# Optimization experiments

Measured on AMD Instinct MI355X. Metric: run time of the kernel, lower is better.

## Reference

```python
import jax, jax.numpy as jnp
import numpy as np

N = 50000        # node_num
E = 1600000      # num edges (avg degree 32)
IN_DIM = 128
OUT_DIM = 64
SLOPE = 0.1      # leaky relu slope_ratio
EPS = 1e-12


def setup_inputs() -> dict:
    key = jax.random.key(0)
    k0, k1, k2, k3 = jax.random.split(key, 4)
    x = jax.random.normal(k0, (N, IN_DIM), dtype=jnp.float32)
    edge_index = jax.random.randint(k1, (2, E), 0, N, dtype=jnp.int64)
    # Linear(in_dim, out_dim) params
    W = jax.random.normal(k2, (OUT_DIM, IN_DIM), dtype=jnp.float32) * (1.0 / np.sqrt(IN_DIM))
    b = jnp.zeros((OUT_DIM,), dtype=jnp.float32)
    # attention vector a: [2*out_dim, 1], kaiming-normal-ish init
    a = jax.random.normal(k3, (2 * OUT_DIM, 1), dtype=jnp.float32) * np.sqrt(2.0 / (2 * OUT_DIM))
    return {"x": x, "edge_index": edge_index, "W": W, "b": b, "a": a}


def reference(x, edge_index, W, b, a):
    # new_embeddings = Linear(x)
    new = x @ W.T + b                          # [N, OUT_DIM]
    src = edge_index[0]
    dst = edge_index[1]
    # cat(new[src], new[dst]) @ a  ==  new[src]@a_src + new[dst]@a_dst (avoids [E, 2*OUT] intermediate)
    a_src = a[:OUT_DIM, 0]                     # [OUT_DIM]
    a_dst = a[OUT_DIM:, 0]                     # [OUT_DIM]
    score = new[src] @ a_src + new[dst] @ a_dst  # [E]
    e = jnp.exp(jax.nn.leaky_relu(score, SLOPE))  # [E]
    # spmm(A, ones) -> per-row sum of edge weights; spmm(A, new) -> weighted aggregation
    row_sum = jax.ops.segment_sum(e, src, num_segments=N)                 # [N]
    results = jax.ops.segment_sum(e[:, None] * new[dst], src, num_segments=N)  # [N, OUT_DIM]
    return results / (row_sum[:, None] + EPS)
```

## Files before the change

### kernel.cpp

```cpp
#include <hip/hip_runtime.h>
#include <hip/hip_bf16.h>

#define NN    50000
#define EE    1600000
#define IND   128
#define OUTD  64
#define SLOPE 0.1f

#define BSH    5
#define BW     32
#define NB     1564
#define NFINE  1568
#define CAP    1408
#define CAPT   6
#define CSH    8
#define NC     196
#define CAP1   8832
#define NBLK1  500
#define CHUNK1 (EE / NBLK1)
#define NSPLIT 4
#define SCAP   (CAP1 / NSPLIT)
#define NLIN   (NN / 16)

typedef __attribute__((ext_vector_type(8))) short short8;
typedef __attribute__((ext_vector_type(4))) float float4v;

union SMem {
    struct {
        ushort xs[16 * 136];
        ushort wt[64 * 136];
        float  newt[16 * 68];
    } lin;
    int h[NC];
};

__global__ __launch_bounds__(256) void fused_lincoarse_kernel(
    const float* __restrict__ x, const float* __restrict__ W,
    const float* __restrict__ bias, const float* __restrict__ a,
    const int* __restrict__ ei, int* __restrict__ gcur1,
    unsigned* __restrict__ ebuf1,
    ushort* __restrict__ nbuf2, float* __restrict__ s_src, float* __restrict__ s_dst)
{
    __shared__ SMem sm;
    const int tid = threadIdx.x;

    if (blockIdx.x < NBLK1) {
        int* h = sm.h;
        for (int i = tid; i < NC; i += 256) h[i] = 0;
        __syncthreads();
        const int base = blockIdx.x * CHUNK1;
        const int4* s4p = (const int4*)(ei + base);
        for (int i = tid; i < CHUNK1 / 4; i += 256) {
            int4 s4 = s4p[i];
            atomicAdd(&h[s4.x >> CSH], 1);
            atomicAdd(&h[s4.y >> CSH], 1);
            atomicAdd(&h[s4.z >> CSH], 1);
            atomicAdd(&h[s4.w >> CSH], 1);
        }
        __syncthreads();
        for (int i = tid; i < NC; i += 256) {
            int c = h[i];
            if (c) h[i] = i * CAP1 + atomicAdd(&gcur1[i * 16], c);
        }
        __syncthreads();
        const int4* d4p = (const int4*)(ei + EE + base);
        for (int i = tid; i < CHUNK1 / 4; i += 256) {
            int4 s4 = s4p[i];
            int4 d4 = d4p[i];
            int p0 = atomicAdd(&h[s4.x >> CSH], 1);
            int p1 = atomicAdd(&h[s4.y >> CSH], 1);
            int p2 = atomicAdd(&h[s4.z >> CSH], 1);
            int p3 = atomicAdd(&h[s4.w >> CSH], 1);
            ebuf1[p0] = ((unsigned)(s4.x & 255) << 16) | (unsigned)d4.x;
            ebuf1[p1] = ((unsigned)(s4.y & 255) << 16) | (unsigned)d4.y;
            ebuf1[p2] = ((unsigned)(s4.z & 255) << 16) | (unsigned)d4.z;
            ebuf1[p3] = ((unsigned)(s4.w & 255) << 16) | (unsigned)d4.w;
        }
        return;
    }

    const int node0 = (blockIdx.x - NBLK1) * 16;
    const float4* W4 = (const float4*)W;
    #pragma unroll
    for (int i = 0; i < 8; ++i) {
        int idx = tid + i * 256;
        float4 wv = W4[idx];
        int n = idx >> 5, k = (idx & 31) * 4;
        ushort4 pk; __hip_bfloat16 h;
        h = __float2bfloat16(wv.x); pk.x = *(ushort*)&h;
        h = __float2bfloat16(wv.y); pk.y = *(ushort*)&h;
        h = __float2bfloat16(wv.z); pk.z = *(ushort*)&h;
        h = __float2bfloat16(wv.w); pk.w = *(ushort*)&h;
        *(ushort4*)&sm.lin.wt[n * 136 + k] = pk;
    }
    const float4* x4 = (const float4*)(x + (size_t)node0 * IND);
    #pragma unroll
    for (int i = 0; i < 2; ++i) {
        int idx = tid + i * 256;
        float4 xv = x4[idx];
        int r = idx >> 5, cc = (idx & 31) * 4;
        ushort4 pk; __hip_bfloat16 h;
        h = __float2bfloat16(xv.x); pk.x = *(ushort*)&h;
        h = __float2bfloat16(xv.y); pk.y = *(ushort*)&h;
        h = __float2bfloat16(xv.z); pk.z = *(ushort*)&h;
        h = __float2bfloat16(xv.w); pk.w = *(ushort*)&h;
        *(ushort4*)&sm.lin.xs[r * 136 + cc] = pk;
    }
    __syncthreads();

    const int w    = tid >> 6;
    const int lane = tid & 63;
    const int q    = lane >> 4;
    const int m16  = lane & 15;
    float4v acc = {0.f, 0.f, 0.f, 0.f};
    #pragma unroll
    for (int kk = 0; kk < IND; kk += 32) {
        short8 af = *(const short8*)&sm.lin.xs[m16 * 136 + kk + q * 8];
        short8 bf = *(const short8*)&sm.lin.wt[(w * 16 + m16) * 136 + kk + q * 8];
        acc = __builtin_amdgcn_mfma_f32_16x16x32_bf16(af, bf, acc, 0, 0, 0);
    }
    const float bv = bias[w * 16 + m16];
    #pragma unroll
    for (int r = 0; r < 4; ++r)
        sm.lin.newt[(q * 4 + r) * 68 + w * 16 + m16] = acc[r] + bv;
    __syncthreads();

    const int nl = tid >> 4;
    const int jg = tid & 15;
    const int j0 = jg * 4;
    float4 va = *(const float4*)&sm.lin.newt[nl * 68 + j0];
    const int n = node0 + nl;
    ushort4 pk;
    { __hip_bfloat16 h;
      h = __float2bfloat16(va.x); pk.x = *(ushort*)&h;
      h = __float2bfloat16(va.y); pk.y = *(ushort*)&h;
      h = __float2bfloat16(va.z); pk.z = *(ushort*)&h;
      h = __float2bfloat16(va.w); pk.w = *(ushort*)&h; }
    *(ushort4*)&nbuf2[(size_t)n * OUTD + j0] = pk;

    float ss = va.x * a[j0]        + va.y * a[j0 + 1]
             + va.z * a[j0 + 2]    + va.w * a[j0 + 3];
    float sd = va.x * a[OUTD + j0]     + va.y * a[OUTD + j0 + 1]
             + va.z * a[OUTD + j0 + 2] + va.w * a[OUTD + j0 + 3];
    #pragma unroll
    for (int m = 1; m < 16; m <<= 1) {
        ss += __shfl_xor(ss, m, 64);
        sd += __shfl_xor(sd, m, 64);
    }
    if (jg == 0) { s_src[n] = ss; s_dst[n] = sd; }
}

__global__ __launch_bounds__(256) void finebin_kernel(
    const unsigned* __restrict__ ebuf1, const int* __restrict__ gcur1,
    int* __restrict__ gcur2, unsigned* __restrict__ ebuf2)
{
    __shared__ unsigned stage[SCAP];
    __shared__ int h[8], lofs[8], grun[8], cur[8];
    const int tid = threadIdx.x;
    const int c   = blockIdx.x >> 2;
    const int sp  = blockIdx.x & 3;
    const int cnt1 = gcur1[c * 16];
    const int seg  = (cnt1 + NSPLIT - 1) / NSPLIT;
    const int lo   = sp * seg;
    const int m    = max(0, min(cnt1, lo + seg) - lo);
    if (tid < 8) h[tid] = 0;
    __syncthreads();
    const unsigned* eb = ebuf1 + (size_t)c * CAP1 + lo;
    for (int i = tid; i < m; i += 256)
        atomicAdd(&h[eb[i] >> 21], 1);
    __syncthreads();
    if (tid == 0) {
        int run = 0;
        #pragma unroll
        for (int f = 0; f < 8; ++f) { lofs[f] = run; run += h[f]; }
    }
    __syncthreads();
    if (tid < 8) {
        cur[tid]  = lofs[tid];
        grun[tid] = atomicAdd(&gcur2[(c * 8 + tid) * 16], h[tid]);
    }
    __syncthreads();
    for (int i = tid; i < m; i += 256) {
        unsigned e = eb[i];
        int pos = atomicAdd(&cur[e >> 21], 1);
        stage[pos] = (((e >> 16) & 31u) << 16) | (e & 0xFFFFu);
    }
    __syncthreads();
    #pragma unroll 1
    for (int f = 0; f < 8; ++f) {
        const int cf = h[f];
        unsigned* dst = ebuf2 + (size_t)(c * 8 + f) * CAP + grun[f];
        const unsigned* sp2 = stage + lofs[f];
        for (int i = tid; i < cf; i += 256) dst[i] = sp2[i];
    }
}

__global__ __launch_bounds__(256) void aggregate_kernel(
    const unsigned* __restrict__ ebuf, const int* __restrict__ gcur,
    const ushort* __restrict__ nbuf2,
    const float* __restrict__ s_src, const float* __restrict__ s_dst,
    float* __restrict__ out)
{
    __shared__ uint2 pairs[CAP];
    __shared__ float ssL[BW];
    __shared__ int cntL[BW], ofs[BW], cur[BW];
    const int tid  = threadIdx.x;
    const int wid  = tid >> 6;
    const int lane = tid & 63;
    const int b    = blockIdx.x;
    const int n0   = b << BSH;
    const uint2* __restrict__ nbufq = (const uint2*)nbuf2;

    if (tid < BW) {
        int n = n0 + tid;
        ssL[tid]  = (n < NN) ? s_src[n] : 0.f;
        cntL[tid] = 0;
    }
    __syncthreads();

    const int cnt = gcur[b * 16];
    const unsigned* eb = ebuf + (size_t)b * CAP;

    unsigned er[CAPT]; float evr[CAPT];
    #pragma unroll
    for (int k = 0; k < CAPT; ++k) {
        int i = tid + k * 256;
        if (i < cnt) {
            unsigned e = eb[i];
            er[k] = e;
            int d  = e & 0xFFFFu;
            int ln = e >> 16;
            float sc = ssL[ln] + s_dst[d];
            float lr = sc > 0.f ? sc : SLOPE * sc;
            evr[k] = __expf(lr);
            atomicAdd(&cntL[ln], 1);
        }
    }
    __syncthreads();

    if (wid == 0) {
        int c = (lane < BW) ? cntL[lane] : 0;
        int sc = c;
        #pragma unroll
        for (int m = 1; m < BW; m <<= 1) {
            int v = __shfl_up(sc, m, 64);
            if (lane >= m) sc += v;
        }
        if (lane < BW) { ofs[lane] = sc - c; cur[lane] = sc - c; }
    }
    __syncthreads();

    #pragma unroll
    for (int k = 0; k < CAPT; ++k) {
        int i = tid + k * 256;
        if (i < cnt) {
            int ln = er[k] >> 16;
            int pos = atomicAdd(&cur[ln], 1);
            pairs[pos] = make_uint2(er[k] & 0xFFFFu, __float_as_uint(evr[k]));
        }
    }
    __syncthreads();

    const int e16 = lane >> 4;
    const int c16 = lane & 15;

    #pragma unroll 1
    for (int t = 0; t < BW / 4; ++t) {
        const int ln  = wid * (BW / 4) + t;
        const int beg = ofs[ln];
        const int len = cntL[ln];

        float a0 = 0.f, a1 = 0.f, a2 = 0.f, a3 = 0.f, es = 0.f;
        int j = 0;
        for (; j + 32 <= len; j += 32) {
            uint2 pA = pairs[beg + j + 0  + e16];
            uint2 pB = pairs[beg + j + 4  + e16];
            uint2 pC = pairs[beg + j + 8  + e16];
            uint2 pD = pairs[beg + j + 12 + e16];
            uint2 pE = pairs[beg + j + 16 + e16];
            uint2 pF = pairs[beg + j + 20 + e16];
            uint2 pG = pairs[beg + j + 24 + e16];
            uint2 pH = pairs[beg + j + 28 + e16];
            uint2 gA = nbufq[pA.x * 16 + c16];
            uint2 gB = nbufq[pB.x * 16 + c16];
            uint2 gC = nbufq[pC.x * 16 + c16];
            uint2 gD = nbufq[pD.x * 16 + c16];
            uint2 gE = nbufq[pE.x * 16 + c16];
            uint2 gF = nbufq[pF.x * 16 + c16];
            uint2 gG = nbufq[pG.x * 16 + c16];
            uint2 gH = nbufq[pH.x * 16 + c16];
            float fA = __uint_as_float(pA.y), fB = __uint_as_float(pB.y);
            float fC = __uint_as_float(pC.y), fD = __uint_as_float(pD.y);
            float fE = __uint_as_float(pE.y), fF = __uint_as_float(pF.y);
            float fG = __uint_as_float(pG.y), fH = __uint_as_float(pH.y);
            es += (fA + fB + fC + fD) + (fE + fF + fG + fH);
            a0 = fmaf(fA, __uint_as_float(gA.x << 16), a0);
            a1 = fmaf(fA, __uint_as_float(gA.x & 0xFFFF0000u), a1);
            a2 = fmaf(fA, __uint_as_float(gA.y << 16), a2);
            a3 = fmaf(fA, __uint_as_float(gA.y & 0xFFFF0000u), a3);
            a0 = fmaf(fB, __uint_as_float(gB.x << 16), a0);
            a1 = fmaf(fB, __uint_as_float(gB.x & 0xFFFF0000u), a1);
            a2 = fmaf(fB, __uint_as_float(gB.y << 16), a2);
            a3 = fmaf(fB, __uint_as_float(gB.y & 0xFFFF0000u), a3);
            a0 = fmaf(fC, __uint_as_float(gC.x << 16), a0);
            a1 = fmaf(fC, __uint_as_float(gC.x & 0xFFFF0000u), a1);
            a2 = fmaf(fC, __uint_as_float(gC.y << 16), a2);
            a3 = fmaf(fC, __uint_as_float(gC.y & 0xFFFF0000u), a3);
            a0 = fmaf(fD, __uint_as_float(gD.x << 16), a0);
            a1 = fmaf(fD, __uint_as_float(gD.x & 0xFFFF0000u), a1);
            a2 = fmaf(fD, __uint_as_float(gD.y << 16), a2);
            a3 = fmaf(fD, __uint_as_float(gD.y & 0xFFFF0000u), a3);
            a0 = fmaf(fE, __uint_as_float(gE.x << 16), a0);
            a1 = fmaf(fE, __uint_as_float(gE.x & 0xFFFF0000u), a1);
            a2 = fmaf(fE, __uint_as_float(gE.y << 16), a2);
            a3 = fmaf(fE, __uint_as_float(gE.y & 0xFFFF0000u), a3);
            a0 = fmaf(fF, __uint_as_float(gF.x << 16), a0);
            a1 = fmaf(fF, __uint_as_float(gF.x & 0xFFFF0000u), a1);
            a2 = fmaf(fF, __uint_as_float(gF.y << 16), a2);
            a3 = fmaf(fF, __uint_as_float(gF.y & 0xFFFF0000u), a3);
            a0 = fmaf(fG, __uint_as_float(gG.x << 16), a0);
            a1 = fmaf(fG, __uint_as_float(gG.x & 0xFFFF0000u), a1);
            a2 = fmaf(fG, __uint_as_float(gG.y << 16), a2);
            a3 = fmaf(fG, __uint_as_float(gG.y & 0xFFFF0000u), a3);
            a0 = fmaf(fH, __uint_as_float(gH.x << 16), a0);
            a1 = fmaf(fH, __uint_as_float(gH.x & 0xFFFF0000u), a1);
            a2 = fmaf(fH, __uint_as_float(gH.y << 16), a2);
            a3 = fmaf(fH, __uint_as_float(gH.y & 0xFFFF0000u), a3);
        }
        for (; j + 16 <= len; j += 16) {
            uint2 pA = pairs[beg + j + 0  + e16];
            uint2 pB = pairs[beg + j + 4  + e16];
            uint2 pC = pairs[beg + j + 8  + e16];
            uint2 pD = pairs[beg + j + 12 + e16];
            uint2 gA = nbufq[pA.x * 16 + c16];
            uint2 gB = nbufq[pB.x * 16 + c16];
            uint2 gC = nbufq[pC.x * 16 + c16];
            uint2 gD = nbufq[pD.x * 16 + c16];
            float fA = __uint_as_float(pA.y), fB = __uint_as_float(pB.y);
            float fC = __uint_as_float(pC.y), fD = __uint_as_float(pD.y);
            es += fA + fB + fC + fD;
            a0 = fmaf(fA, __uint_as_float(gA.x << 16), a0);
            a1 = fmaf(fA, __uint_as_float(gA.x & 0xFFFF0000u), a1);
            a2 = fmaf(fA, __uint_as_float(gA.y << 16), a2);
            a3 = fmaf(fA, __uint_as_float(gA.y & 0xFFFF0000u), a3);
            a0 = fmaf(fB, __uint_as_float(gB.x << 16), a0);
            a1 = fmaf(fB, __uint_as_float(gB.x & 0xFFFF0000u), a1);
            a2 = fmaf(fB, __uint_as_float(gB.y << 16), a2);
            a3 = fmaf(fB, __uint_as_float(gB.y & 0xFFFF0000u), a3);
            a0 = fmaf(fC, __uint_as_float(gC.x << 16), a0);
            a1 = fmaf(fC, __uint_as_float(gC.x & 0xFFFF0000u), a1);
            a2 = fmaf(fC, __uint_as_float(gC.y << 16), a2);
            a3 = fmaf(fC, __uint_as_float(gC.y & 0xFFFF0000u), a3);
            a0 = fmaf(fD, __uint_as_float(gD.x << 16), a0);
            a1 = fmaf(fD, __uint_as_float(gD.x & 0xFFFF0000u), a1);
            a2 = fmaf(fD, __uint_as_float(gD.y << 16), a2);
            a3 = fmaf(fD, __uint_as_float(gD.y & 0xFFFF0000u), a3);
        }
        for (; j < len; j += 4) {
            int idx = j + e16;
            uint2 p = pairs[beg + min(idx, len - 1)];
            float f = (idx < len) ? __uint_as_float(p.y) : 0.f;
            uint2 g = nbufq[p.x * 16 + c16];
            es += f;
            a0 = fmaf(f, __uint_as_float(g.x << 16), a0);
            a1 = fmaf(f, __uint_as_float(g.x & 0xFFFF0000u), a1);
            a2 = fmaf(f, __uint_as_float(g.y << 16), a2);
            a3 = fmaf(f, __uint_as_float(g.y & 0xFFFF0000u), a3);
        }
        es += __shfl_xor(es, 16, 64); es += __shfl_xor(es, 32, 64);
        a0 += __shfl_xor(a0, 16, 64); a0 += __shfl_xor(a0, 32, 64);
        a1 += __shfl_xor(a1, 16, 64); a1 += __shfl_xor(a1, 32, 64);
        a2 += __shfl_xor(a2, 16, 64); a2 += __shfl_xor(a2, 32, 64);
        a3 += __shfl_xor(a3, 16, 64); a3 += __shfl_xor(a3, 32, 64);
        const int n = n0 + ln;
        if (e16 == 0 && n < NN) {
            float inv = 1.f / (es + 1e-12f);
            float4 o = make_float4(a0 * inv, a1 * inv, a2 * inv, a3 * inv);
            *(float4*)&out[(size_t)n * OUTD + c16 * 4] = o;
        }
    }
}

extern "C" void kernel_launch(void* const* d_in, const int* in_sizes, int n_in,
                              void* d_out, int out_size, void* d_ws, size_t ws_size,
                              hipStream_t stream) {
    const float* x  = (const float*)d_in[0];
    const int*   ei = (const int*)d_in[1];
    const float* W  = (const float*)d_in[2];
    const float* b  = (const float*)d_in[3];
    const float* a  = (const float*)d_in[4];
    float* out = (float*)d_out;

    ushort*   nbuf2 = (ushort*)d_ws;
    float*    s_src = (float*)(nbuf2 + (size_t)NN * OUTD);
    float*    s_dst = s_src + NN;
    int*      gcur1 = (int*)(s_dst + NN);
    int*      gcur2 = gcur1 + NC * 16;
    unsigned* ebuf1 = (unsigned*)(gcur2 + NFINE * 16);
    unsigned* ebuf2 = ebuf1 + (size_t)NC * CAP1;

    hipMemsetAsync(gcur1, 0, (NC + NFINE) * 16 * sizeof(int), stream);
    fused_lincoarse_kernel<<<NBLK1 + NLIN, 256, 0, stream>>>(
        x, W, b, a, ei, gcur1, ebuf1, nbuf2, s_src, s_dst);
    finebin_kernel<<<NC * NSPLIT, 256, 0, stream>>>(ebuf1, gcur1, gcur2, ebuf2);
    aggregate_kernel<<<NB, 256, 0, stream>>>(ebuf2, gcur2, nbuf2, s_src, s_dst, out);
}
```

Measured before the change: 145.3 us.

## Bin edges directly into fine 32-node buckets, dropping the two-pass finebin kernel

The coarse-then-fine two-stage edge binning is replaced by a single pass in the fused kernel that histograms edges straight into the 1568 fine buckets and scatters them into the per-bucket buffers that aggregate consumes. This removes the finebin launch, the intermediate ebuf1 write and read, and one global counter array. Source int4 loads are also cached in registers between the count and scatter passes. In exchange each block touches many more shared histogram entries and global atomics (1568 instead of 196 per block), and global writes become more scattered.

Result: slower. 171.1 us (+17.7%).

```diff
diff --git a/kernel.cpp b/kernel.cpp
--- a/kernel.cpp
+++ b/kernel.cpp
@@ -10,16 +10,11 @@
 #define BSH    5
 #define BW     32
 #define NB     1564
-#define NFINE  1568
+#define NFB    1568
 #define CAP    1408
 #define CAPT   6
-#define CSH    8
-#define NC     196
-#define CAP1   8832
 #define NBLK1  500
 #define CHUNK1 (EE / NBLK1)
-#define NSPLIT 4
-#define SCAP   (CAP1 / NSPLIT)
 #define NLIN   (NN / 16)
 
 typedef __attribute__((ext_vector_type(8))) short short8;
@@ -31,14 +26,14 @@
         ushort wt[64 * 136];
         float  newt[16 * 68];
     } lin;
-    int h[NC];
+    int h[NFB];
 };
 
 __global__ __launch_bounds__(256) void fused_lincoarse_kernel(
     const float* __restrict__ x, const float* __restrict__ W,
     const float* __restrict__ bias, const float* __restrict__ a,
-    const int* __restrict__ ei, int* __restrict__ gcur1,
-    unsigned* __restrict__ ebuf1,
+    const int* __restrict__ ei, int* __restrict__ gcur,
+    unsigned* __restrict__ ebuf,
     ushort* __restrict__ nbuf2, float* __restrict__ s_src, float* __restrict__ s_dst)
 {
     __shared__ SMem sm;
@@ -46,35 +41,45 @@
 
     if (blockIdx.x < NBLK1) {
         int* h = sm.h;
-        for (int i = tid; i < NC; i += 256) h[i] = 0;
+        for (int i = tid; i < NFB; i += 256) h[i] = 0;
         __syncthreads();
         const int base = blockIdx.x * CHUNK1;
         const int4* s4p = (const int4*)(ei + base);
-        for (int i = tid; i < CHUNK1 / 4; i += 256) {
-            int4 s4 = s4p[i];
-            atomicAdd(&h[s4.x >> CSH], 1);
-            atomicAdd(&h[s4.y >> CSH], 1);
-            atomicAdd(&h[s4.z >> CSH], 1);
-            atomicAdd(&h[s4.w >> CSH], 1);
+        int4 sst[4];
+        #pragma unroll
+        for (int k = 0; k < 4; ++k) {
+            int i = tid + k * 256;
+            if (i < CHUNK1 / 4) {
+                int4 s4 = s4p[i];
+                sst[k] = s4;
+                atomicAdd(&h[s4.x >> BSH], 1);
+                atomicAdd(&h[s4.y >> BSH], 1);
+                atomicAdd(&h[s4.z >> BSH], 1);
+                atomicAdd(&h[s4.w >> BSH], 1);
+            }
         }
         __syncthreads();
-        for (int i = tid; i < NC; i += 256) {
+        for (int i = tid; i < NFB; i += 256) {
             int c = h[i];
-            if (c) h[i] = i * CAP1 + atomicAdd(&gcur1[i * 16], c);
+            if (c) h[i] = i * CAP + atomicAdd(&gcur[i * 16], c);
         }
         __syncthreads();
         const int4* d4p = (const int4*)(ei + EE + base);
-        for (int i = tid; i < CHUNK1 / 4; i += 256) {
-            int4 s4 = s4p[i];
-            int4 d4 = d4p[i];
-            int p0 = atomicAdd(&h[s4.x >> CSH], 1);
-            int p1 = atomicAdd(&h[s4.y >> CSH], 1);
-            int p2 = atomicAdd(&h[s4.z >> CSH], 1);
-            int p3 = atomicAdd(&h[s4.w >> CSH], 1);
-            ebuf1[p0] = ((unsigned)(s4.x & 255) << 16) | (unsigned)d4.x;
-            ebuf1[p1] = ((unsigned)(s4.y & 255) << 16) | (unsigned)d4.y;
-            ebuf1[p2] = ((unsigned)(s4.z & 255) << 16) | (unsigned)d4.z;
-            ebuf1[p3] = ((unsigned)(s4.w & 255) << 16) | (unsigned)d4.w;
+        #pragma unroll
+        for (int k = 0; k < 4; ++k) {
+            int i = tid + k * 256;
+            if (i < CHUNK1 / 4) {
+                int4 s4 = sst[k];
+                int4 d4 = d4p[i];
+                int p0 = atomicAdd(&h[s4.x >> BSH], 1);
+                int p1 = atomicAdd(&h[s4.y >> BSH], 1);
+                int p2 = atomicAdd(&h[s4.z >> BSH], 1);
+                int p3 = atomicAdd(&h[s4.w >> BSH], 1);
+                ebuf[p0] = ((unsigned)(s4.x & 31) << 16) | (unsigned)d4.x;
+                ebuf[p1] = ((unsigned)(s4.y & 31) << 16) | (unsigned)d4.y;
+                ebuf[p2] = ((unsigned)(s4.z & 31) << 16) | (unsigned)d4.z;
+                ebuf[p3] = ((unsigned)(s4.w & 31) << 16) | (unsigned)d4.w;
+            }
         }
         return;
     }
@@ -148,51 +153,6 @@
         sd += __shfl_xor(sd, m, 64);
     }
     if (jg == 0) { s_src[n] = ss; s_dst[n] = sd; }
-}
-
-__global__ __launch_bounds__(256) void finebin_kernel(
-    const unsigned* __restrict__ ebuf1, const int* __restrict__ gcur1,
-    int* __restrict__ gcur2, unsigned* __restrict__ ebuf2)
-{
-    __shared__ unsigned stage[SCAP];
-    __shared__ int h[8], lofs[8], grun[8], cur[8];
-    const int tid = threadIdx.x;
-    const int c   = blockIdx.x >> 2;
-    const int sp  = blockIdx.x & 3;
-    const int cnt1 = gcur1[c * 16];
-    const int seg  = (cnt1 + NSPLIT - 1) / NSPLIT;
-    const int lo   = sp * seg;
-    const int m    = max(0, min(cnt1, lo + seg) - lo);
-    if (tid < 8) h[tid] = 0;
-    __syncthreads();
-    const unsigned* eb = ebuf1 + (size_t)c * CAP1 + lo;
-    for (int i = tid; i < m; i += 256)
-        atomicAdd(&h[eb[i] >> 21], 1);
-    __syncthreads();
-    if (tid == 0) {
-        int run = 0;
-        #pragma unroll
-        for (int f = 0; f < 8; ++f) { lofs[f] = run; run += h[f]; }
-    }
-    __syncthreads();
-    if (tid < 8) {
-        cur[tid]  = lofs[tid];
-        grun[tid] = atomicAdd(&gcur2[(c * 8 + tid) * 16], h[tid]);
-    }
-    __syncthreads();
-    for (int i = tid; i < m; i += 256) {
-        unsigned e = eb[i];
-        int pos = atomicAdd(&cur[e >> 21], 1);
-        stage[pos] = (((e >> 16) & 31u) << 16) | (e & 0xFFFFu);
-    }
-    __syncthreads();
-    #pragma unroll 1
-    for (int f = 0; f < 8; ++f) {
-        const int cf = h[f];
-        unsigned* dst = ebuf2 + (size_t)(c * 8 + f) * CAP + grun[f];
-        const unsigned* sp2 = stage + lofs[f];
-        for (int i = tid; i < cf; i += 256) dst[i] = sp2[i];
-    }
 }
 
 __global__ __launch_bounds__(256) void aggregate_kernel(
@@ -394,14 +354,11 @@
     ushort*   nbuf2 = (ushort*)d_ws;
     float*    s_src = (float*)(nbuf2 + (size_t)NN * OUTD);
     float*    s_dst = s_src + NN;
-    int*      gcur1 = (int*)(s_dst + NN);
-    int*      gcur2 = gcur1 + NC * 16;
-    unsigned* ebuf1 = (unsigned*)(gcur2 + NFINE * 16);
-    unsigned* ebuf2 = ebuf1 + (size_t)NC * CAP1;
-
-    hipMemsetAsync(gcur1, 0, (NC + NFINE) * 16 * sizeof(int), stream);
+    int*      gcur2 = (int*)(s_dst + NN);
+    unsigned* ebuf2 = (unsigned*)(gcur2 + NFB * 16);
+
+    hipMemsetAsync(gcur2, 0, NFB * 16 * sizeof(int), stream);
     fused_lincoarse_kernel<<<NBLK1 + NLIN, 256, 0, stream>>>(
-        x, W, b, a, ei, gcur1, ebuf1, nbuf2, s_src, s_dst);
-    finebin_kernel<<<NC * NSPLIT, 256, 0, stream>>>(ebuf1, gcur1, gcur2, ebuf2);
+        x, W, b, a, ei, gcur2, ebuf2, nbuf2, s_src, s_dst);
     aggregate_kernel<<<NB, 256, 0, stream>>>(ebuf2, gcur2, nbuf2, s_src, s_dst, out);
 }
```

## Move linear projection from coarse-bin kernel into fine-bin kernel, double coarse blocks

Applied to the files above, without the earlier changes.

Coarse binning now runs in its own kernel with twice as many blocks. Each thread keeps its src indices in registers between the histogram pass and the scatter pass instead of reloading them. The linear projection blocks are merged into the fine-binning kernel, so the small fine-bin workload overlaps with the GEMM instead of running as a separate, underfilled launch. This changes how work is balanced across the three launches. It also raises the number of global atomics on the coarse counters, since more blocks each reserve space.

Result: slower. 155.2 us (+6.8%).

```diff
diff --git a/kernel.cpp b/kernel.cpp
--- a/kernel.cpp
+++ b/kernel.cpp
@@ -16,56 +16,51 @@
 #define CSH    8
 #define NC     196
 #define CAP1   8832
-#define NBLK1  500
+#define NBLK1  1000
 #define CHUNK1 (EE / NBLK1)
 #define NSPLIT 4
 #define SCAP   (CAP1 / NSPLIT)
+#define NFBB   (NC * NSPLIT)
 #define NLIN   (NN / 16)
 
 typedef __attribute__((ext_vector_type(8))) short short8;
 typedef __attribute__((ext_vector_type(4))) float float4v;
 
-union SMem {
-    struct {
-        ushort xs[16 * 136];
-        ushort wt[64 * 136];
-        float  newt[16 * 68];
-    } lin;
-    int h[NC];
-};
-
-__global__ __launch_bounds__(256) void fused_lincoarse_kernel(
-    const float* __restrict__ x, const float* __restrict__ W,
-    const float* __restrict__ bias, const float* __restrict__ a,
+__global__ __launch_bounds__(256) void bin_kernel(
     const int* __restrict__ ei, int* __restrict__ gcur1,
-    unsigned* __restrict__ ebuf1,
-    ushort* __restrict__ nbuf2, float* __restrict__ s_src, float* __restrict__ s_dst)
+    unsigned* __restrict__ ebuf1)
 {
-    __shared__ SMem sm;
+    __shared__ int h[NC];
     const int tid = threadIdx.x;
-
-    if (blockIdx.x < NBLK1) {
-        int* h = sm.h;
-        for (int i = tid; i < NC; i += 256) h[i] = 0;
-        __syncthreads();
-        const int base = blockIdx.x * CHUNK1;
-        const int4* s4p = (const int4*)(ei + base);
-        for (int i = tid; i < CHUNK1 / 4; i += 256) {
+    for (int i = tid; i < NC; i += 256) h[i] = 0;
+    __syncthreads();
+    const int base = blockIdx.x * CHUNK1;
+    const int4* s4p = (const int4*)(ei + base);
+    int4 sst[2];
+    #pragma unroll
+    for (int k = 0; k < 2; ++k) {
+        int i = tid + k * 256;
+        if (i < CHUNK1 / 4) {
             int4 s4 = s4p[i];
+            sst[k] = s4;
             atomicAdd(&h[s4.x >> CSH], 1);
             atomicAdd(&h[s4.y >> CSH], 1);
             atomicAdd(&h[s4.z >> CSH], 1);
             atomicAdd(&h[s4.w >> CSH], 1);
         }
-        __syncthreads();
-        for (int i = tid; i < NC; i += 256) {
-            int c = h[i];
-            if (c) h[i] = i * CAP1 + atomicAdd(&gcur1[i * 16], c);
-        }
-        __syncthreads();
-        const int4* d4p = (const int4*)(ei + EE + base);
-        for (int i = tid; i < CHUNK1 / 4; i += 256) {
-            int4 s4 = s4p[i];
+    }
+    __syncthreads();
+    for (int i = tid; i < NC; i += 256) {
+        int c = h[i];
+        if (c) h[i] = i * CAP1 + atomicAdd(&gcur1[i * 16], c);
+    }
+    __syncthreads();
+    const int4* d4p = (const int4*)(ei + EE + base);
+    #pragma unroll
+    for (int k = 0; k < 2; ++k) {
+        int i = tid + k * 256;
+        if (i < CHUNK1 / 4) {
+            int4 s4 = sst[k];
             int4 d4 = d4p[i];
             int p0 = atomicAdd(&h[s4.x >> CSH], 1);
             int p1 = atomicAdd(&h[s4.y >> CSH], 1);
@@ -76,10 +71,75 @@
             ebuf1[p2] = ((unsigned)(s4.z & 255) << 16) | (unsigned)d4.z;
             ebuf1[p3] = ((unsigned)(s4.w & 255) << 16) | (unsigned)d4.w;
         }
+    }
+}
+
+union SMem2 {
+    struct {
+        unsigned stage[SCAP];
+        int h[8], lofs[8], grun[8], cur[8];
+    } fb;
+    struct {
+        ushort xs[16 * 136];
+        ushort wt[64 * 136];
+        float  newt[16 * 68];
+    } lin;
+};
+
+__global__ __launch_bounds__(256) void finelin_kernel(
+    const float* __restrict__ x, const float* __restrict__ W,
+    const float* __restrict__ bias, const float* __restrict__ a,
+    const unsigned* __restrict__ ebuf1, const int* __restrict__ gcur1,
+    int* __restrict__ gcur2, unsigned* __restrict__ ebuf2,
+    ushort* __restrict__ nbuf2, float* __restrict__ s_src, float* __restrict__ s_dst)
+{
+    __shared__ SMem2 sm;
+    const int tid = threadIdx.x;
+
+    if (blockIdx.x < NFBB) {
+        unsigned* stage = sm.fb.stage;
+        int* h = sm.fb.h; int* lofs = sm.fb.lofs;
+        int* grun = sm.fb.grun; int* cur = sm.fb.cur;
+        const int c   = blockIdx.x >> 2;
+        const int sp  = blockIdx.x & 3;
+        const int cnt1 = gcur1[c * 16];
+        const int seg  = (cnt1 + NSPLIT - 1) / NSPLIT;
+        const int lo   = sp * seg;
+        const int m    = max(0, min(cnt1, lo + seg) - lo);
+        if (tid < 8) h[tid] = 0;
+        __syncthreads();
+        const unsigned* eb = ebuf1 + (size_t)c * CAP1 + lo;
+        for (int i = tid; i < m; i += 256)
+            atomicAdd(&h[eb[i] >> 21], 1);
+        __syncthreads();
+        if (tid == 0) {
+            int run = 0;
+            #pragma unroll
+            for (int f = 0; f < 8; ++f) { lofs[f] = run; run += h[f]; }
+        }
+        __syncthreads();
+        if (tid < 8) {
+            cur[tid]  = lofs[tid];
+            grun[tid] = atomicAdd(&gcur2[(c * 8 + tid) * 16], h[tid]);
+        }
+        __syncthreads();
+        for (int i = tid; i < m; i += 256) {
+            unsigned e = eb[i];
+            int pos = atomicAdd(&cur[e >> 21], 1);
+            stage[pos] = (((e >> 16) & 31u) << 16) | (e & 0xFFFFu);
+        }
+        __syncthreads();
+        #pragma unroll 1
+        for (int f = 0; f < 8; ++f) {
+            const int cf = h[f];
+            unsigned* dst = ebuf2 + (size_t)(c * 8 + f) * CAP + grun[f];
+            const unsigned* sp2 = stage + lofs[f];
+            for (int i = tid; i < cf; i += 256) dst[i] = sp2[i];
+        }
         return;
     }
 
-    const int node0 = (blockIdx.x - NBLK1) * 16;
+    const int node0 = (blockIdx.x - NFBB) * 16;
     const float4* W4 = (const float4*)W;
     #pragma unroll
     for (int i = 0; i < 8; ++i) {
@@ -148,51 +208,6 @@
         sd += __shfl_xor(sd, m, 64);
     }
     if (jg == 0) { s_src[n] = ss; s_dst[n] = sd; }
-}
-
-__global__ __launch_bounds__(256) void finebin_kernel(
-    const unsigned* __restrict__ ebuf1, const int* __restrict__ gcur1,
-    int* __restrict__ gcur2, unsigned* __restrict__ ebuf2)
-{
-    __shared__ unsigned stage[SCAP];
-    __shared__ int h[8], lofs[8], grun[8], cur[8];
-    const int tid = threadIdx.x;
-    const int c   = blockIdx.x >> 2;
-    const int sp  = blockIdx.x & 3;
-    const int cnt1 = gcur1[c * 16];
-    const int seg  = (cnt1 + NSPLIT - 1) / NSPLIT;
-    const int lo   = sp * seg;
-    const int m    = max(0, min(cnt1, lo + seg) - lo);
-    if (tid < 8) h[tid] = 0;
-    __syncthreads();
-    const unsigned* eb = ebuf1 + (size_t)c * CAP1 + lo;
-    for (int i = tid; i < m; i += 256)
-        atomicAdd(&h[eb[i] >> 21], 1);
-    __syncthreads();
-    if (tid == 0) {
-        int run = 0;
-        #pragma unroll
-        for (int f = 0; f < 8; ++f) { lofs[f] = run; run += h[f]; }
-    }
-    __syncthreads();
-    if (tid < 8) {
-        cur[tid]  = lofs[tid];
-        grun[tid] = atomicAdd(&gcur2[(c * 8 + tid) * 16], h[tid]);
-    }
-    __syncthreads();
-    for (int i = tid; i < m; i += 256) {
-        unsigned e = eb[i];
-        int pos = atomicAdd(&cur[e >> 21], 1);
-        stage[pos] = (((e >> 16) & 31u) << 16) | (e & 0xFFFFu);
-    }
-    __syncthreads();
-    #pragma unroll 1
-    for (int f = 0; f < 8; ++f) {
-        const int cf = h[f];
-        unsigned* dst = ebuf2 + (size_t)(c * 8 + f) * CAP + grun[f];
-        const unsigned* sp2 = stage + lofs[f];
-        for (int i = tid; i < cf; i += 256) dst[i] = sp2[i];
-    }
 }
 
 __global__ __launch_bounds__(256) void aggregate_kernel(
@@ -400,8 +415,8 @@
     unsigned* ebuf2 = ebuf1 + (size_t)NC * CAP1;
 
     hipMemsetAsync(gcur1, 0, (NC + NFINE) * 16 * sizeof(int), stream);
-    fused_lincoarse_kernel<<<NBLK1 + NLIN, 256, 0, stream>>>(
-        x, W, b, a, ei, gcur1, ebuf1, nbuf2, s_src, s_dst);
-    finebin_kernel<<<NC * NSPLIT, 256, 0, stream>>>(ebuf1, gcur1, gcur2, ebuf2);
+    bin_kernel<<<NBLK1, 256, 0, stream>>>(ei, gcur1, ebuf1);
+    finelin_kernel<<<NFBB + NLIN, 256, 0, stream>>>(
+        x, W, b, a, ebuf1, gcur1, gcur2, ebuf2, nbuf2, s_src, s_dst);
     aggregate_kernel<<<NB, 256, 0, stream>>>(ebuf2, gcur2, nbuf2, s_src, s_dst, out);
 }
```
